# Optimization experiments

Measured on AMD Instinct MI355X. Metric: run time of the kernel, lower is better.

## Reference

```python
import jax, jax.numpy as jnp
import numpy as np

N_NODES = 1_000_000
N_EDGES = 10_000_000
HIDDEN = 8
N_GRAPHS = 64


def _gcn_conv(h_in, W, b, src, dst, deg_inv_sqrt, n_nodes):
    """One PyG GCNConv: symmetric-normalized aggregation over (A + I)."""
    h = h_in @ W  # [N, out]
    norm = deg_inv_sqrt[src] * deg_inv_sqrt[dst]  # [E]
    msgs = h[src] * norm[:, None]  # gather + scale, [E, out]
    out = jax.ops.segment_sum(msgs, dst, num_segments=n_nodes)  # scatter-add
    out = out + h * (deg_inv_sqrt * deg_inv_sqrt)[:, None]  # self-loop term
    return out + b


def setup_inputs() -> dict:
    key = jax.random.key(0)
    ks = jax.random.split(key, 12)
    x = jax.random.uniform(ks[0], (N_NODES, 1), dtype=jnp.float32)
    edge_index = jax.random.randint(ks[1], (2, N_EDGES), 0, N_NODES, dtype=jnp.int64)
    indices = jax.random.randint(ks[2], (N_GRAPHS,), 0, N_NODES, dtype=jnp.int64)
    # Glorot-ish init for GCNConv linear layers (no bias in lin; GCNConv bias separate)
    W1 = jax.random.normal(ks[3], (1, HIDDEN), dtype=jnp.float32) * (1.0 / np.sqrt(1))
    W2 = jax.random.normal(ks[4], (HIDDEN, HIDDEN), dtype=jnp.float32) * (1.0 / np.sqrt(HIDDEN))
    W3 = jax.random.normal(ks[5], (HIDDEN, HIDDEN), dtype=jnp.float32) * (1.0 / np.sqrt(HIDDEN))
    W4 = jax.random.normal(ks[6], (HIDDEN, HIDDEN), dtype=jnp.float32) * (1.0 / np.sqrt(HIDDEN))
    b1 = jnp.zeros((HIDDEN,), jnp.float32)
    b2 = jnp.zeros((HIDDEN,), jnp.float32)
    b3 = jnp.zeros((HIDDEN,), jnp.float32)
    b4 = jnp.zeros((HIDDEN,), jnp.float32)
    return {"x": x, "edge_index": edge_index, "indices": indices,
            "W1": W1, "b1": b1, "W2": W2, "b2": b2,
            "W3": W3, "b3": b3, "W4": W4, "b4": b4}


def reference(x, edge_index, indices, W1, b1, W2, b2, W3, b3, W4, b4):
    n_nodes = x.shape[0]
    src, dst = edge_index[0], edge_index[1]
    # degree under A + I (symmetric GCN normalization)
    deg = jax.ops.segment_sum(jnp.ones_like(dst, dtype=x.dtype), dst,
                              num_segments=n_nodes) + 1.0
    deg_inv_sqrt = jax.lax.rsqrt(deg)
    h = x
    for W, b, last in ((W1, b1, False), (W2, b2, False), (W3, b3, False), (W4, b4, True)):
        h = _gcn_conv(h, W, b, src, dst, deg_inv_sqrt, n_nodes)
        if not last:
            h = jax.nn.relu(h)
    return h[indices]  # one node embedding per batched graph, [B, 8]
```

## Files before the change

### kernel.cpp

```cpp
#include <hip/hip_runtime.h>
#include <hip/hip_fp16.h>

#define TPB 256
#define STPB 512
#define BTPB 512
#define NBK 256
#define BNODES 4096
#define QNODES 1024
#define CH 6144
#define CAPB 45056
#define QSTG 12288
#define CAP_L 262144

typedef unsigned int uv4 __attribute__((ext_vector_type(4)));
union H8 { uv4 u; __half2 h2[4]; };

__global__ void init_tails(int* __restrict__ tails) {
    tails[threadIdx.x] = threadIdx.x * CAPB;
}

__global__ __launch_bounds__(STPB) void scatter_sort(const int* __restrict__ dst,
                                                     const int* __restrict__ src,
                                                     int* __restrict__ tails,
                                                     unsigned* __restrict__ bdata, int nE) {
    __shared__ unsigned      stage[CH];
    __shared__ unsigned char bkt[CH];
    __shared__ int cnt[NBK], sstart[NBK], cur[NBK], cbase[NBK];
    __shared__ int wsum[STPB / 64];
    int t = threadIdx.x;
    long base = (long)blockIdx.x * CH;
    int m = (int)(((long)nE - base < CH) ? (nE - base) : CH);
    if (t < NBK) cnt[t] = 0;
    __syncthreads();
    for (int k = t * 4; k < m; k += STPB * 4) {
        if (k + 3 < m) {
            int4 d4 = *(const int4*)(dst + base + k);
            atomicAdd(&cnt[d4.x >> 12], 1);
            atomicAdd(&cnt[d4.y >> 12], 1);
            atomicAdd(&cnt[d4.z >> 12], 1);
            atomicAdd(&cnt[d4.w >> 12], 1);
        } else {
            int ke = (k + 4 < m) ? (k + 4) : m;
            for (int kk = k; kk < ke; ++kk)
                atomicAdd(&cnt[dst[base + kk] >> 12], 1);
        }
    }
    __syncthreads();
    int v = 0, incl = 0;
    if (t < NBK) {
        v = cnt[t]; incl = v;
#pragma unroll
        for (int o = 1; o < 64; o <<= 1) {
            int u = __shfl_up(incl, o, 64);
            if ((t & 63) >= o) incl += u;
        }
        if ((t & 63) == 63) wsum[t >> 6] = incl;
    }
    __syncthreads();
    if (t < NBK) {
        int wadd = 0;
#pragma unroll
        for (int w = 0; w < 3; ++w) wadd += (w < (t >> 6)) ? wsum[w] : 0;
        int ex = incl - v + wadd;
        sstart[t] = ex;
        cur[t] = ex;
        cbase[t] = v ? atomicAdd(&tails[t], v) : 0;
    }
    __syncthreads();
    for (int k = t * 4; k < m; k += STPB * 4) {
        if (k + 3 < m) {
            int4 d4 = *(const int4*)(dst + base + k);
            int4 s4 = *(const int4*)(src + base + k);
            { int b = d4.x >> 12; int pos = atomicAdd(&cur[b], 1);
              stage[pos] = ((unsigned)(d4.x & 4095) << 20) | (unsigned)s4.x; bkt[pos] = (unsigned char)b; }
            { int b = d4.y >> 12; int pos = atomicAdd(&cur[b], 1);
              stage[pos] = ((unsigned)(d4.y & 4095) << 20) | (unsigned)s4.y; bkt[pos] = (unsigned char)b; }
            { int b = d4.z >> 12; int pos = atomicAdd(&cur[b], 1);
              stage[pos] = ((unsigned)(d4.z & 4095) << 20) | (unsigned)s4.z; bkt[pos] = (unsigned char)b; }
            { int b = d4.w >> 12; int pos = atomicAdd(&cur[b], 1);
              stage[pos] = ((unsigned)(d4.w & 4095) << 20) | (unsigned)s4.w; bkt[pos] = (unsigned char)b; }
        } else {
            int ke = (k + 4 < m) ? (k + 4) : m;
            for (int kk = k; kk < ke; ++kk) {
                int d = dst[base + kk], s = src[base + kk];
                int b = d >> 12; int pos = atomicAdd(&cur[b], 1);
                stage[pos] = ((unsigned)(d & 4095) << 20) | (unsigned)s; bkt[pos] = (unsigned char)b;
            }
        }
    }
    __syncthreads();
    for (int k = t; k < m; k += STPB) {
        int b = bkt[k];
        bdata[cbase[b] + (k - sstart[b])] = stage[k];
    }
}

__global__ void bucket_prefix(const int* __restrict__ tails, int* __restrict__ P) {
    __shared__ int lds[NBK];
    int t = threadIdx.x;
    int c = tails[t] - t * CAPB;
    lds[t] = c;
    __syncthreads();
    for (int off = 1; off < NBK; off <<= 1) {
        int u = (t >= off) ? lds[t - off] : 0;
        __syncthreads();
        lds[t] += u;
        __syncthreads();
    }
    P[t] = lds[t] - c;
    if (t == NBK - 1) P[NBK] = lds[t];
}

__global__ __launch_bounds__(BTPB) void quarter_csr(const unsigned* __restrict__ bdata,
                                                    const int* __restrict__ tails,
                                                    const int* __restrict__ P,
                                                    const float* __restrict__ x,
                                                    const float* __restrict__ W1,
                                                    int* __restrict__ rowptr,
                                                    __half* __restrict__ hs,
                                                    int* __restrict__ col, int n) {
    __shared__ int      off[QNODES];
    __shared__ int      wsum[BTPB / 64];
    __shared__ int      wred[BTPB / 64];
    __shared__ int      sQb, sTot;
    __shared__ unsigned stg[QSTG];
    int bid = blockIdx.x, t = threadIdx.x;
    int b = bid >> 2, q = bid & 3;
    int e0 = b * CAPB, e1 = tails[b];
    for (int j = t; j < QNODES; j += BTPB) off[j] = 0;
    __syncthreads();
    int before = 0;
    for (int k = e0 + t * 4; k < e1; k += BTPB * 4) {
        if (k + 3 < e1) {
            uv4 p4 = *(const uv4*)(bdata + k);
#pragma unroll
            for (int z = 0; z < 4; ++z) {
                int j = (int)(p4[z] >> 20); int jq = j >> 10;
                if (jq == q) atomicAdd(&off[j & 1023], 1);
                before += (jq < q) ? 1 : 0;
            }
        } else {
            for (int kk = k; kk < e1; ++kk) {
                int j = (int)(bdata[kk] >> 20); int jq = j >> 10;
                if (jq == q) atomicAdd(&off[j & 1023], 1);
                before += (jq < q) ? 1 : 0;
            }
        }
    }
#pragma unroll
    for (int o = 32; o > 0; o >>= 1) before += __shfl_down(before, o, 64);
    if ((t & 63) == 0) wred[t >> 6] = before;
    __syncthreads();
    if (t == 0) {
        int s = 0;
#pragma unroll
        for (int w = 0; w < BTPB / 64; ++w) s += wred[w];
        sQb = s;
    }
    int a = off[2 * t], c = off[2 * t + 1];
    int s2 = a + c;
    int incl = s2;
#pragma unroll
    for (int o = 1; o < 64; o <<= 1) {
        int u = __shfl_up(incl, o, 64);
        if ((t & 63) >= o) incl += u;
    }
    if ((t & 63) == 63) wsum[t >> 6] = incl;
    __syncthreads();
    int wadd = 0;
#pragma unroll
    for (int w = 0; w < BTPB / 64 - 1; ++w) wadd += (w < (t >> 6)) ? wsum[w] : 0;
    int pex = incl - s2 + wadd;
    off[2 * t]     = pex;
    off[2 * t + 1] = pex + a;
    if (t == BTPB - 1) sTot = pex + s2;
    int PbQb = P[b] + sQb;
    {
        int node0 = (b << 12) + (q << 10) + 2 * t;
        float4 w0 = ((const float4*)W1)[0];
        float4 w1 = ((const float4*)W1)[1];
        if (node0 + 1 < n) {
            int2 rp; rp.x = PbQb + pex; rp.y = PbQb + pex + a;
            *(int2*)(rowptr + node0) = rp;
            float2 xv = *(const float2*)(x + node0);
            float dv0 = rsqrtf((float)a + 1.0f);
            float dv1 = rsqrtf((float)c + 1.0f);
            float xd0 = xv.x * dv0, xd1 = xv.y * dv1;
            H8 o0, o1;
            o0.h2[0] = __floats2half2_rn(xd0 * w0.x, xd0 * w0.y);
            o0.h2[1] = __floats2half2_rn(xd0 * w0.z, xd0 * w0.w);
            o0.h2[2] = __floats2half2_rn(xd0 * w1.x, xd0 * w1.y);
            o0.h2[3] = __floats2half2_rn(xd0 * w1.z, xd0 * w1.w);
            o1.h2[0] = __floats2half2_rn(xd1 * w0.x, xd1 * w0.y);
            o1.h2[1] = __floats2half2_rn(xd1 * w0.z, xd1 * w0.w);
            o1.h2[2] = __floats2half2_rn(xd1 * w1.x, xd1 * w1.y);
            o1.h2[3] = __floats2half2_rn(xd1 * w1.z, xd1 * w1.w);
            ((uv4*)hs)[node0]     = o0.u;
            ((uv4*)hs)[node0 + 1] = o1.u;
        } else {
            if (node0 <= n)     rowptr[node0]     = PbQb + pex;
            if (node0 + 1 <= n) rowptr[node0 + 1] = PbQb + pex + a;
            if (node0 < n) {
                float dv = rsqrtf((float)a + 1.0f);
                float xd = x[node0] * dv;
                H8 o;
                o.h2[0] = __floats2half2_rn(xd * w0.x, xd * w0.y);
                o.h2[1] = __floats2half2_rn(xd * w0.z, xd * w0.w);
                o.h2[2] = __floats2half2_rn(xd * w1.x, xd * w1.y);
                o.h2[3] = __floats2half2_rn(xd * w1.z, xd * w1.w);
                ((uv4*)hs)[node0] = o.u;
            }
        }
    }
    __syncthreads();
    for (int k = e0 + t * 4; k < e1; k += BTPB * 4) {
        if (k + 3 < e1) {
            uv4 p4 = *(const uv4*)(bdata + k);
#pragma unroll
            for (int z = 0; z < 4; ++z) {
                int j = (int)(p4[z] >> 20);
                if ((j >> 10) == q) {
                    int pos = atomicAdd(&off[j & 1023], 1);
                    stg[pos] = p4[z] & 0xFFFFFu;
                }
            }
        } else {
            for (int kk = k; kk < e1; ++kk) {
                unsigned p = bdata[kk];
                int j = (int)(p >> 20);
                if ((j >> 10) == q) {
                    int pos = atomicAdd(&off[j & 1023], 1);
                    stg[pos] = p & 0xFFFFFu;
                }
            }
        }
    }
    __syncthreads();
    int tot = sTot;
    for (int k = t; k < tot; k += BTPB)
        col[PbQb + k] = (int)stg[k];
}

__global__ void seed_mark_q(const int* __restrict__ idx, int B, int* __restrict__ mark,
                            int* __restrict__ L, int* __restrict__ qq) {
    int t = threadIdx.x;
    if (t < B) {
        int u = idx[t];
        if (atomicCAS(&mark[u], 0, 1) == 0)
            L[atomicAdd(&qq[7], 1)] = u;
    }
}

__global__ __launch_bounds__(TPB) void expand_f(int* __restrict__ L, int* __restrict__ qq,
                                                int tier,
                                                const int* __restrict__ rowptr,
                                                const int* __restrict__ col,
                                                int* __restrict__ mark) {
    int hi = qq[7];
    int stride = gridDim.x * blockDim.x;
    for (int r = blockIdx.x * blockDim.x + threadIdx.x; r < hi; r += stride) {
        int u = L[r];
        if (mark[u] != tier - 1) continue;
        int e0 = rowptr[u], e1 = rowptr[u + 1];
        for (int k = e0; k < e1; ++k) {
            int s = col[k];
            if (mark[s] == 0 && atomicCAS(&mark[s], 0, tier) == 0)
                L[atomicAdd(&qq[7], 1)] = s;
        }
    }
}

__global__ void pull_tier(const int* __restrict__ L, const int* __restrict__ qq,
                          int tagMax, const int* __restrict__ mark,
                          const int* __restrict__ rowptr, const int* __restrict__ col,
                          const __half* __restrict__ hs_in, const float* __restrict__ bias,
                          const float* __restrict__ W, __half* __restrict__ hs_out) {
    int r = blockIdx.x * blockDim.x + threadIdx.x;
    if (r >= qq[7]) return;
    int u = L[r];
    if (mark[u] > tagMax) return;
    const uv4* hv = (const uv4*)hs_in;
    H8 p; p.u = hv[u];
    float2 a0 = __half22float2(p.h2[0]);
    float2 a1 = __half22float2(p.h2[1]);
    float2 a2 = __half22float2(p.h2[2]);
    float2 a3 = __half22float2(p.h2[3]);
    int s = rowptr[u], e = rowptr[u + 1];
    for (int k = s; k < e; ++k) {
        H8 q; q.u = hv[col[k]];
        float2 b0 = __half22float2(q.h2[0]);
        float2 b1 = __half22float2(q.h2[1]);
        float2 b2 = __half22float2(q.h2[2]);
        float2 b3 = __half22float2(q.h2[3]);
        a0.x += b0.x; a0.y += b0.y; a1.x += b1.x; a1.y += b1.y;
        a2.x += b2.x; a2.y += b2.y; a3.x += b3.x; a3.y += b3.y;
    }
    float d = rsqrtf((float)(e - s) + 1.0f);
    float t[8] = {a0.x * d, a0.y * d, a1.x * d, a1.y * d,
                  a2.x * d, a2.y * d, a3.x * d, a3.y * d};
#pragma unroll
    for (int k = 0; k < 8; ++k) {
        float v = t[k] + bias[k];
        t[k] = v > 0.0f ? v : 0.0f;
    }
    float h[8];
#pragma unroll
    for (int j = 0; j < 8; ++j) {
        float acc = 0.0f;
#pragma unroll
        for (int k = 0; k < 8; ++k) acc += t[k] * W[k * 8 + j];
        h[j] = acc * d;
    }
    H8 o;
    o.h2[0] = __floats2half2_rn(h[0], h[1]);
    o.h2[1] = __floats2half2_rn(h[2], h[3]);
    o.h2[2] = __floats2half2_rn(h[4], h[5]);
    o.h2[3] = __floats2half2_rn(h[6], h[7]);
    ((uv4*)hs_out)[u] = o.u;
}

__global__ void pull_final(const int* __restrict__ idx, int B,
                           const int* __restrict__ rowptr, const int* __restrict__ col,
                           const __half* __restrict__ hs_in,
                           const float* __restrict__ b4, float* __restrict__ out) {
    int t = blockIdx.x * blockDim.x + threadIdx.x;
    if (t >= B) return;
    int u = idx[t];
    const uv4* hv = (const uv4*)hs_in;
    H8 p; p.u = hv[u];
    float2 a0 = __half22float2(p.h2[0]);
    float2 a1 = __half22float2(p.h2[1]);
    float2 a2 = __half22float2(p.h2[2]);
    float2 a3 = __half22float2(p.h2[3]);
    int s = rowptr[u], e = rowptr[u + 1];
    for (int k = s; k < e; ++k) {
        H8 q; q.u = hv[col[k]];
        float2 b0 = __half22float2(q.h2[0]);
        float2 b1 = __half22float2(q.h2[1]);
        float2 b2 = __half22float2(q.h2[2]);
        float2 b3 = __half22float2(q.h2[3]);
        a0.x += b0.x; a0.y += b0.y; a1.x += b1.x; a1.y += b1.y;
        a2.x += b2.x; a2.y += b2.y; a3.x += b3.x; a3.y += b3.y;
    }
    float d = rsqrtf((float)(e - s) + 1.0f);
    float* op = out + (size_t)t * 8;
    op[0] = a0.x * d + b4[0]; op[1] = a0.y * d + b4[1];
    op[2] = a1.x * d + b4[2]; op[3] = a1.y * d + b4[3];
    op[4] = a2.x * d + b4[4]; op[5] = a2.y * d + b4[5];
    op[6] = a3.x * d + b4[6]; op[7] = a3.y * d + b4[7];
}

extern "C" void kernel_launch(void* const* d_in, const int* in_sizes, int n_in,
                              void* d_out, int out_size, void* d_ws, size_t ws_size,
                              hipStream_t stream) {
    const float* x   = (const float*)d_in[0];
    const int*   ei  = (const int*)d_in[1];
    const int*   idx = (const int*)d_in[2];
    const float* W1  = (const float*)d_in[3];
    const float* b1  = (const float*)d_in[4];
    const float* W2  = (const float*)d_in[5];
    const float* b2  = (const float*)d_in[6];
    const float* W3  = (const float*)d_in[7];
    const float* b3  = (const float*)d_in[8];
    const float* W4  = (const float*)d_in[9];
    const float* b4  = (const float*)d_in[10];

    const int n = in_sizes[0];
    const int E = in_sizes[1] / 2;
    const int B = in_sizes[2];

    const int* src = ei;
    const int* dst = ei + E;

    const int NB = (n + BNODES - 1) / BNODES;

    size_t o_mark = 0;
    size_t o_rp   = o_mark + (size_t)n;
    size_t o_hsA  = o_rp   + (size_t)n + 8;
    size_t o_L    = o_hsA  + (size_t)n * 4;
    size_t o_col  = o_L    + CAP_L;
    size_t o_bd   = o_col  + (size_t)E;
    size_t o_sm   = o_bd   + (size_t)NB * CAPB;

    int*      mark   = (int*)d_ws + o_mark;
    int*      rowptr = (int*)d_ws + o_rp;
    __half*   hsA    = (__half*)((int*)d_ws + o_hsA);
    int*      L      = (int*)d_ws + o_L;
    int*      col    = (int*)d_ws + o_col;
    unsigned* bdata  = (unsigned*)((int*)d_ws + o_bd);
    __half*   hsB    = (__half*)bdata;
    int*      tails  = (int*)d_ws + o_sm;
    int*      P      = tails + NBK + 8;
    int*      qq     = P + NBK + 8;

    const int gs  = (int)(((long)E + CH - 1) / CH);
    const int nb2 = CAP_L / TPB;

    (void)hipMemsetAsync(mark, 0, (size_t)n * sizeof(int), stream);
    (void)hipMemsetAsync(qq, 0, 16 * sizeof(int), stream);
    init_tails<<<1, NBK, 0, stream>>>(tails);

    scatter_sort<<<gs, STPB, 0, stream>>>(dst, src, tails, bdata, E);

    bucket_prefix<<<1, NBK, 0, stream>>>(tails, P);
    quarter_csr<<<NB * 4, BTPB, 0, stream>>>(bdata, tails, P, x, W1, rowptr, hsA, col, n);

    seed_mark_q<<<1, 64, 0, stream>>>(idx, B, mark, L, qq);
    expand_f<<<64, TPB, 0, stream>>>(L, qq, 2, rowptr, col, mark);
    expand_f<<<128, TPB, 0, stream>>>(L, qq, 3, rowptr, col, mark);
    expand_f<<<256, TPB, 0, stream>>>(L, qq, 4, rowptr, col, mark);

    pull_tier<<<nb2, TPB, 0, stream>>>(L, qq, 4, mark, rowptr, col, hsA, b1, W2, hsB);
    pull_tier<<<nb2, TPB, 0, stream>>>(L, qq, 3, mark, rowptr, col, hsB, b2, W3, hsA);
    pull_tier<<<nb2, TPB, 0, stream>>>(L, qq, 2, mark, rowptr, col, hsA, b3, W4, hsB);
    pull_final<<<1, 64, 0, stream>>>(idx, B, rowptr, col, hsB, b4, (float*)d_out);
}
```

Before: 421.3 us.

## Drop init/prefix kernels, fold bucket prefix into CSR build, warp-aggregate queue appends

Tails now hold per-bucket counts zeroed by a single memset, replacing the init_tails kernel and the separate qq memset. The bucket_prefix kernel is removed: each quarter_csr block computes its own bucket prefix with a block reduction over tails. Block IDs are remapped so that consecutive buckets spread across the eight XCDs. In expand_f, a wavefront ballot lets one lane per wave do the queue-append atomic instead of one per lane. The changes cut two kernel launches and reduce atomic contention, at the cost of a small redundant reduction in every CSR block.

```diff
diff --git a/kernel.cpp b/kernel.cpp
--- a/kernel.cpp
+++ b/kernel.cpp
@@ -14,10 +14,6 @@
 
 typedef unsigned int uv4 __attribute__((ext_vector_type(4)));
 union H8 { uv4 u; __half2 h2[4]; };
-
-__global__ void init_tails(int* __restrict__ tails) {
-    tails[threadIdx.x] = threadIdx.x * CAPB;
-}
 
 __global__ __launch_bounds__(STPB) void scatter_sort(const int* __restrict__ dst,
                                                      const int* __restrict__ src,
@@ -64,7 +60,7 @@
         int ex = incl - v + wadd;
         sstart[t] = ex;
         cur[t] = ex;
-        cbase[t] = v ? atomicAdd(&tails[t], v) : 0;
+        cbase[t] = v ? (t * CAPB + atomicAdd(&tails[t], v)) : 0;
     }
     __syncthreads();
     for (int k = t * 4; k < m; k += STPB * 4) {
@@ -95,40 +91,37 @@
     }
 }
 
-__global__ void bucket_prefix(const int* __restrict__ tails, int* __restrict__ P) {
-    __shared__ int lds[NBK];
-    int t = threadIdx.x;
-    int c = tails[t] - t * CAPB;
-    lds[t] = c;
-    __syncthreads();
-    for (int off = 1; off < NBK; off <<= 1) {
-        int u = (t >= off) ? lds[t - off] : 0;
-        __syncthreads();
-        lds[t] += u;
-        __syncthreads();
-    }
-    P[t] = lds[t] - c;
-    if (t == NBK - 1) P[NBK] = lds[t];
-}
-
 __global__ __launch_bounds__(BTPB) void quarter_csr(const unsigned* __restrict__ bdata,
                                                     const int* __restrict__ tails,
-                                                    const int* __restrict__ P,
                                                     const float* __restrict__ x,
                                                     const float* __restrict__ W1,
                                                     int* __restrict__ rowptr,
                                                     __half* __restrict__ hs,
-                                                    int* __restrict__ col, int n) {
+                                                    int* __restrict__ col, int n, int NB) {
     __shared__ int      off[QNODES];
     __shared__ int      wsum[BTPB / 64];
-    __shared__ int      wred[BTPB / 64];
-    __shared__ int      sQb, sTot;
+    __shared__ int      wredQ[BTPB / 64];
+    __shared__ int      wredP[BTPB / 64];
+    __shared__ int      sQb, sTot, sPb;
     __shared__ unsigned stg[QSTG];
     int bid = blockIdx.x, t = threadIdx.x;
-    int b = bid >> 2, q = bid & 3;
-    int e0 = b * CAPB, e1 = tails[b];
+    int xcd = bid & 7, slot = bid >> 3;
+    int b = (slot >> 2) * 8 + xcd;
+    int q = slot & 3;
+    if (b >= NB) return;
+    int e0 = b * CAPB, e1 = e0 + tails[b];
     for (int j = t; j < QNODES; j += BTPB) off[j] = 0;
-    __syncthreads();
+    int partial = (t < b) ? tails[t] : 0;
+#pragma unroll
+    for (int o = 32; o > 0; o >>= 1) partial += __shfl_down(partial, o, 64);
+    if ((t & 63) == 0) wredP[t >> 6] = partial;
+    __syncthreads();
+    if (t == 0) {
+        int s = 0;
+#pragma unroll
+        for (int w = 0; w < BTPB / 64; ++w) s += wredP[w];
+        sPb = s;
+    }
     int before = 0;
     for (int k = e0 + t * 4; k < e1; k += BTPB * 4) {
         if (k + 3 < e1) {
@@ -149,12 +142,12 @@
     }
 #pragma unroll
     for (int o = 32; o > 0; o >>= 1) before += __shfl_down(before, o, 64);
-    if ((t & 63) == 0) wred[t >> 6] = before;
+    if ((t & 63) == 0) wredQ[t >> 6] = before;
     __syncthreads();
     if (t == 0) {
         int s = 0;
 #pragma unroll
-        for (int w = 0; w < BTPB / 64; ++w) s += wred[w];
+        for (int w = 0; w < BTPB / 64; ++w) s += wredQ[w];
         sQb = s;
     }
     int a = off[2 * t], c = off[2 * t + 1];
@@ -174,7 +167,7 @@
     off[2 * t]     = pex;
     off[2 * t + 1] = pex + a;
     if (t == BTPB - 1) sTot = pex + s2;
-    int PbQb = P[b] + sQb;
+    int PbQb = sPb + sQb;
     {
         int node0 = (b << 12) + (q << 10) + 2 * t;
         float4 w0 = ((const float4*)W1)[0];
@@ -258,14 +251,26 @@
                                                 int* __restrict__ mark) {
     int hi = qq[7];
     int stride = gridDim.x * blockDim.x;
+    int lane = threadIdx.x & 63;
     for (int r = blockIdx.x * blockDim.x + threadIdx.x; r < hi; r += stride) {
         int u = L[r];
         if (mark[u] != tier - 1) continue;
         int e0 = rowptr[u], e1 = rowptr[u + 1];
         for (int k = e0; k < e1; ++k) {
             int s = col[k];
-            if (mark[s] == 0 && atomicCAS(&mark[s], 0, tier) == 0)
-                L[atomicAdd(&qq[7], 1)] = s;
+            bool ok = (mark[s] == 0) && (atomicCAS(&mark[s], 0, tier) == 0);
+            unsigned long long msk = __ballot(ok);
+            if (msk) {
+                int leader = __builtin_ctzll(msk);
+                int cntw = __builtin_popcountll(msk);
+                int basep = 0;
+                if (lane == leader) basep = atomicAdd(&qq[7], cntw);
+                basep = __shfl(basep, leader, 64);
+                if (ok) {
+                    int myoff = __builtin_popcountll(msk & ((1ull << lane) - 1ull));
+                    L[basep + myoff] = s;
+                }
+            }
         }
     }
 }
@@ -390,20 +395,18 @@
     unsigned* bdata  = (unsigned*)((int*)d_ws + o_bd);
     __half*   hsB    = (__half*)bdata;
     int*      tails  = (int*)d_ws + o_sm;
-    int*      P      = tails + NBK + 8;
-    int*      qq     = P + NBK + 8;
+    int*      qq     = tails + NBK;
 
     const int gs  = (int)(((long)E + CH - 1) / CH);
     const int nb2 = CAP_L / TPB;
+    const int gq  = ((NB + 7) / 8) * 32;
 
     (void)hipMemsetAsync(mark, 0, (size_t)n * sizeof(int), stream);
-    (void)hipMemsetAsync(qq, 0, 16 * sizeof(int), stream);
-    init_tails<<<1, NBK, 0, stream>>>(tails);
+    (void)hipMemsetAsync(tails, 0, (NBK + 16) * sizeof(int), stream);
 
     scatter_sort<<<gs, STPB, 0, stream>>>(dst, src, tails, bdata, E);
 
-    bucket_prefix<<<1, NBK, 0, stream>>>(tails, P);
-    quarter_csr<<<NB * 4, BTPB, 0, stream>>>(bdata, tails, P, x, W1, rowptr, hsA, col, n);
+    quarter_csr<<<gq, BTPB, 0, stream>>>(bdata, tails, x, W1, rowptr, hsA, col, n, NB);
 
     seed_mark_q<<<1, 64, 0, stream>>>(idx, B, mark, L, qq);
     expand_f<<<64, TPB, 0, stream>>>(L, qq, 2, rowptr, col, mark);
```

Result: faster. 410.6 us (-2.5%).
